# Performance work log

Measured on AMD Instinct MI355X. Metric: run time of the kernel, lower is better.

The kernel has to match this reference:

```python
import jax, jax.numpy as jnp
import numpy as np

NEG_SLOPE = 0.2


def gatv2(x, src, dst, eattr, Wl, bl, Wr, br, We, att, bias, concat):
    # GATv2Conv (PyG semantics): message j->i, softmax over incoming edges of target i.
    n = x.shape[0]
    H, C = att.shape
    xl = (x @ Wl + bl).reshape(n, H, C)   # source transform lin_l
    xr = (x @ Wr + br).reshape(n, H, C)   # target transform lin_r
    xe = (eattr @ We).reshape(-1, H, C)   # edge transform lin_edge (no bias)
    g = jax.nn.leaky_relu(xl[src] + xr[dst] + xe, NEG_SLOPE)  # [E,H,C]
    e = jnp.einsum('ehc,hc->eh', g, att)                      # [E,H]
    m = jax.ops.segment_max(e, dst, num_segments=n)
    a = jnp.exp(e - m[dst])
    s = jax.ops.segment_sum(a, dst, num_segments=n)
    alpha = a / (s[dst] + 1e-16)                              # [E,H]
    out = jax.ops.segment_sum(alpha[:, :, None] * xl[src], dst, num_segments=n)
    out = out.reshape(n, H * C) if concat else out.mean(axis=1)
    return out + bias, alpha


def add_self_loops(src, dst, eattr, n):
    # PyG default: add_self_loops=True, fill_value='mean' for edge_attr
    loop = jnp.arange(n, dtype=src.dtype)
    fill = jnp.broadcast_to(eattr.mean(axis=0, keepdims=True), (n, eattr.shape[1]))
    return (jnp.concatenate([src, loop]), jnp.concatenate([dst, loop]),
            jnp.concatenate([eattr, fill], axis=0))


def setup_inputs() -> dict:
    key = jax.random.key(0)
    ks = iter(jax.random.split(key, 64))
    B, N, D = 4, 2048, 256
    n = B * N
    E = 131072
    H, C1 = 4, 64  # conv1: heads=4, out=hidden//heads=64 (concat -> 256)
    C2 = 256       # conv2: heads=4, out=256, concat=False (mean)
    IN1 = 770

    def rn(shape, s=0.05):
        return jax.random.normal(next(ks), shape, dtype=jnp.float32) * s

    inp = {
        'h': rn((B, N, D), 1.0), 'c_temp': rn((B, N, D), 1.0),
        'c_stereo': rn((B, N, D), 1.0), 'e_proj': rn((B, N, 2), 1.0),
        'f_Lt': rn((B, N, D), 1.0),
        'edges': jax.random.randint(next(ks), (2, E), 0, n, dtype=jnp.int64),
        'edge_attr': rn((E, 1), 1.0),
        # conv1
        'Wl1': rn((IN1, H * C1)), 'bl1': jnp.zeros((H * C1,), jnp.float32),
        'Wr1': rn((IN1, H * C1)), 'br1': jnp.zeros((H * C1,), jnp.float32),
        'We1': rn((1, H * C1)), 'att1': rn((H, C1)),
        'bias1': jnp.zeros((H * C1,), jnp.float32),
        # conv2
        'Wl2': rn((D, H * C2)), 'bl2': jnp.zeros((H * C2,), jnp.float32),
        'Wr2': rn((D, H * C2)), 'br2': jnp.zeros((H * C2,), jnp.float32),
        'We2': rn((1, H * C2)), 'att2': rn((H, C2)),
        'bias2': jnp.zeros((C2,), jnp.float32),
        # GRUCell ([in, 3H] layout; gate order r,z,n as in torch)
        'Wih': rn((D, 3 * D)), 'bih': jnp.zeros((3 * D,), jnp.float32),
        'Whh': rn((D, 3 * D)), 'bhh': jnp.zeros((3 * D,), jnp.float32),
        # heads
        'rW1': rn((D, 256)), 'rb1': jnp.zeros((256,), jnp.float32),
        'rW2': rn((256, 2)), 'rb2': jnp.zeros((2,), jnp.float32),
        'wW1': rn((D, 256)), 'wb1': jnp.zeros((256,), jnp.float32),
        'wW2': rn((256, 2)), 'wb2': jnp.zeros((2,), jnp.float32),
        'pW1': rn((D, 128)), 'pb1': jnp.zeros((128,), jnp.float32),
        'pW2': rn((128, 1)), 'pb2': jnp.zeros((1,), jnp.float32),
        'dW1': rn((D, 128)), 'db1': jnp.zeros((128,), jnp.float32),
        'dW2': rn((128, 1)), 'db2': jnp.zeros((1,), jnp.float32),
    }
    return inp


def reference(h, c_temp, c_stereo, e_proj, f_Lt, edges, edge_attr,
              Wl1, bl1, Wr1, br1, We1, att1, bias1,
              Wl2, bl2, Wr2, br2, We2, att2, bias2,
              Wih, bih, Whh, bhh,
              rW1, rb1, rW2, rb2, wW1, wb1, wW2, wb2,
              pW1, pb1, pW2, pb2, dW1, db1, dW2, db2):
    B, N, D = f_Lt.shape
    n = B * N
    x = jnp.concatenate([c_temp, c_stereo, e_proj, f_Lt], axis=-1).reshape(n, -1)

    src, dst, ea = add_self_loops(edges[0], edges[1], edge_attr, n)
    x1, _ = gatv2(x, src, dst, ea, Wl1, bl1, Wr1, br1, We1, att1, bias1, concat=True)
    x1 = jax.nn.relu(x1)
    x2, alpha = gatv2(x1, src, dst, ea, Wl2, bl2, Wr2, br2, We2, att2, bias2, concat=False)

    # GRUCell
    hf = h.reshape(n, -1)
    gi = x2 @ Wih + bih
    gh = hf @ Whh + bhh
    ir, iz, inew = jnp.split(gi, 3, axis=-1)
    hr, hz, hnew = jnp.split(gh, 3, axis=-1)
    r_g = jax.nn.sigmoid(ir + hr)
    z_g = jax.nn.sigmoid(iz + hz)
    n_g = jnp.tanh(inew + r_g * hnew)
    h_new = ((1.0 - z_g) * n_g + z_g * hf).reshape(B, N, D)

    res = jax.nn.relu(h_new @ rW1 + rb1) @ rW2 + rb2
    w = jax.nn.sigmoid(jax.nn.relu(h_new @ wW1 + wb1) @ wW2 + wb2)
    a_p = jax.nn.softplus(jax.nn.relu(h_new @ pW1 + pb1) @ pW2 + pb2).mean(axis=1)
    a_d = jax.nn.softplus(jax.nn.relu(h_new @ dW1 + db1) @ dW2 + db2)
    return (h_new, res, w, a_p, a_d)
```

## Files before the change

kernel.cpp:

```cpp
#include <hip/hip_runtime.h>
#include <hip/hip_bf16.h>
#include <cstdint>
#include <cstddef>

#define N_NODES 8192
#define E_RAW   131072
#define E_TOT   (E_RAW + N_NODES)
#define HEADS   4

typedef __attribute__((ext_vector_type(8))) __bf16 bf16x8;
typedef __attribute__((ext_vector_type(4))) float f32x4;
typedef __attribute__((ext_vector_type(2))) float f32x2;

__device__ __forceinline__ void gload_lds16(const void* g, void* lds) {
  __builtin_amdgcn_global_load_lds(
      (const __attribute__((address_space(1))) unsigned int*)g,
      (__attribute__((address_space(3))) unsigned int*)lds, 16, 0, 0);
}

__device__ __forceinline__ float bfbits2f(unsigned short u) {
  return __uint_as_float((unsigned)u << 16);
}
__device__ __forceinline__ unsigned short f2bfbits(float f) {
  __hip_bfloat16 b = __float2bfloat16(f);
  return *(unsigned short*)&b;
}
__device__ __forceinline__ f32x2 unpk2(unsigned u) {
  return (f32x2){__uint_as_float(u << 16), __uint_as_float(u & 0xffff0000u)};
}
__device__ __forceinline__ unsigned char f32_to_fp8(float v) {
  int r = __builtin_amdgcn_cvt_pk_fp8_f32(v, v, 0, false);
  return (unsigned char)(r & 0xff);
}

__device__ __forceinline__ int eSrc(const int* __restrict__ src, int e) {
  return (e < E_RAW) ? src[e] : (e - E_RAW);
}
__device__ __forceinline__ int eDst(const int* __restrict__ dst, int e) {
  return (e < E_RAW) ? dst[e] : (e - E_RAW);
}


__global__ __launch_bounds__(256) void prep_kernel(
    const float* __restrict__ ct, const float* __restrict__ cs,
    const float* __restrict__ ep, const float* __restrict__ fl,
    const float* __restrict__ h, const float* __restrict__ ea,
    const float* bl1, const float* br1, const float* bl2, const float* br2,
    const float* rb1, const float* wb1, const float* pb1, const float* db1,
    __hip_bfloat16* __restrict__ x, __hip_bfloat16* __restrict__ Hb,
    float* __restrict__ MP, int* __restrict__ icnt_ipos,
    float* B1, float* B2, float* BH) {
  int blk = blockIdx.x;
  int tid = threadIdx.x;
  if (blk < 8192) {
    int i = blk;
    for (int j = tid; j < 832; j += 256) {
      float v;
      if (j < 256)      v = ct[(size_t)i * 256 + j];
      else if (j < 512) v = cs[(size_t)i * 256 + (j - 256)];
      else if (j < 514) v = ep[(size_t)i * 2 + (j - 512)];
      else if (j < 770) v = fl[(size_t)i * 256 + (j - 514)];
      else              v = 0.f;
      x[(size_t)i * 832 + j] = __float2bfloat16(v);
    }
  } else if (blk < 9216) {
    size_t base = ((size_t)(blk - 8192) * 256 + tid) * 8;
    float4 a = *(const float4*)(h + base);
    float4 b = *(const float4*)(h + base + 4);
    unsigned short o[8];
    o[0]=f2bfbits(a.x); o[1]=f2bfbits(a.y); o[2]=f2bfbits(a.z); o[3]=f2bfbits(a.w);
    o[4]=f2bfbits(b.x); o[5]=f2bfbits(b.y); o[6]=f2bfbits(b.z); o[7]=f2bfbits(b.w);
    *(uint4*)((unsigned short*)Hb + base) = *(uint4*)o;
  } else if (blk < 9472) {
    __shared__ float sm[256];
    int bb = blk - 9216;
    float acc = 0.f;
    for (int i = bb * 256 + tid; i < E_RAW; i += 256 * 256) acc += ea[i];
    sm[tid] = acc; __syncthreads();
    for (int s = 128; s; s >>= 1) { if (tid < s) sm[tid] += sm[tid + s]; __syncthreads(); }
    if (tid == 0) MP[bb] = sm[0];
  } else if (blk < 9536) {
    int i = (blk - 9472) * 256 + tid;
    if (i < 2 * N_NODES) icnt_ipos[i] = 0;
  } else {
    int i = (blk - 9536) * 256 + tid;
    if (i < 512) B1[i] = (i < 256) ? bl1[i] : br1[i - 256];
    else if (i < 2560) { int k = i - 512; B2[k] = (k < 1024) ? bl2[k] : br2[k - 1024]; }
    else if (i < 3328) {
      int k = i - 2560;
      BH[k] = (k < 256) ? rb1[k] : (k < 512) ? wb1[k - 256] : (k < 640) ? pb1[k - 512] : db1[k - 640];
    }
  }
}


__global__ void csr_count(const int* __restrict__ dst, int* __restrict__ cnt) {
  int e = blockIdx.x * blockDim.x + threadIdx.x;
  if (e < E_TOT) atomicAdd(&cnt[eDst(dst, e)], 1);
}

__global__ __launch_bounds__(1024) void csr_scan(const int* __restrict__ cnt,
                                                 int* __restrict__ off,
                                                 float* __restrict__ MP) {
  __shared__ int part[1024];
  __shared__ float sm[256];
  int t = threadIdx.x;
  if (t < 256) sm[t] = MP[t];
  __syncthreads();
  for (int s = 128; s; s >>= 1) { if (t < s) sm[t] += sm[t + s]; __syncthreads(); }
  if (t == 0) MP[256] = sm[0] * (1.f / (float)E_RAW);
  int base = t * 8;
  int loc[8];
  int s = 0;
#pragma unroll
  for (int i = 0; i < 8; ++i) { loc[i] = s; s += cnt[base + i]; }
  part[t] = s; __syncthreads();
  for (int d = 1; d < 1024; d <<= 1) {
    int v = (t >= d) ? part[t - d] : 0;
    __syncthreads();
    part[t] += v;
    __syncthreads();
  }
  int pre = (t == 0) ? 0 : part[t - 1];
#pragma unroll
  for (int i = 0; i < 8; ++i) off[base + i] = pre + loc[i];
  if (t == 1023) off[8192] = part[1023];
}

__global__ void csr_fill(const int* __restrict__ src, const int* __restrict__ dst,
                         const float* __restrict__ ea, const float* __restrict__ eamean,
                         const int* __restrict__ off, int* __restrict__ pos,
                         int* __restrict__ srcn, float* __restrict__ eav) {
  int e = blockIdx.x * blockDim.x + threadIdx.x;
  if (e >= E_TOT) return;
  int d = eDst(dst, e);
  int p = off[d] + atomicAdd(&pos[d], 1);
  srcn[p] = eSrc(src, e);
  eav[p] = (e < E_RAW) ? ea[e] : eamean[0];
}


__global__ __launch_bounds__(256) void wt_all(
    const float* w0, const float* w1, const float* w2, const float* w3,
    const float* w4, const float* w5, const float* w6, const float* w7,
    const float* w8, const float* w9,
    __hip_bfloat16* WT1, __hip_bfloat16* WT2, __hip_bfloat16* WTih,
    __hip_bfloat16* WThh, __hip_bfloat16* WTh) {
  const int cum[10] = {208, 416, 672, 928, 1120, 1312, 1376, 1440, 1472, 1504};
  const int Kt[10]  = {770, 770, 256, 256, 256, 256, 256, 256, 256, 256};
  const int Nt[10]  = {256, 256, 1024, 1024, 768, 768, 256, 256, 128, 128};
  const int KPt[10] = {832, 832, 256, 256, 256, 256, 256, 256, 256, 256};
  const int n0t[10] = {0, 256, 0, 1024, 0, 0, 0, 256, 512, 640};
  int job = 0;
  while (blockIdx.x >= (unsigned)cum[job]) ++job;
  int lb = blockIdx.x - (job ? cum[job - 1] : 0);
  int K = Kt[job], N = Nt[job], KP = KPt[job], n0 = n0t[job];
  int tilesX = KP >> 5;
  int k0 = (lb % tilesX) * 32, nb = (lb / tilesX) * 32;
  const float* W;
  switch (job) {
    case 0: W = w0; break; case 1: W = w1; break; case 2: W = w2; break;
    case 3: W = w3; break; case 4: W = w4; break; case 5: W = w5; break;
    case 6: W = w6; break; case 7: W = w7; break; case 8: W = w8; break;
    default: W = w9; break;
  }
  __hip_bfloat16* WT = (job < 2) ? WT1 : (job < 4) ? WT2 : (job == 4) ? WTih
                       : (job == 5) ? WThh : WTh;
  __shared__ float sm[32][33];
  int tx = threadIdx.x & 31, ty = threadIdx.x >> 5;
  for (int yy = ty; yy < 32; yy += 8) {
    int k = k0 + yy, n = nb + tx;
    sm[yy][tx] = (k < K && n < N) ? W[(size_t)k * N + n] : 0.f;
  }
  __syncthreads();
  for (int yy = ty; yy < 32; yy += 8) {
    int n = nb + yy, k = k0 + tx;
    if (n < N) WT[(size_t)(n0 + n) * KP + k] = __float2bfloat16(sm[tx][yy]);
  }
}


template <int OUT>
__global__ __launch_bounds__(512) void mfma_gemm(
    const __hip_bfloat16* __restrict__ A, const __hip_bfloat16* __restrict__ BT,
    const float* __restrict__ bias, void* __restrict__ Cout, int KP, int N,
    unsigned char* __restrict__ Cfp8) {
  __shared__ uint4 AsBuf[1024];
  __shared__ uint4 BsBuf[1024];
  char* Asc = (char*)AsBuf;
  char* Bsc = (char*)BsBuf;
  int tid = threadIdx.x;
  int lane = tid & 63;
  int wid = tid >> 6;
  int wr = wid >> 1;
  int wc = wid & 1;
  int bm = blockIdx.y * 128;
  int bn = blockIdx.x * 128;
  f32x4 acc[2][4];
#pragma unroll
  for (int i = 0; i < 2; ++i)
#pragma unroll
    for (int j = 0; j < 4; ++j) acc[i][j] = (f32x4){0.f, 0.f, 0.f, 0.f};

  int nK = KP >> 6;
  for (int kt = 0; kt < nK; ++kt) {
    int k0 = kt * 64;
#pragma unroll
    for (int i = 0; i < 2; ++i) {
      int p = i * 512 + tid;
      int row = p >> 3, cc = p & 7;
      int sc = cc ^ (row & 7);
      gload_lds16(A + (size_t)(bm + row) * KP + k0 + sc * 8, Asc + p * 16);
      gload_lds16(BT + (size_t)(bn + row) * KP + k0 + sc * 8, Bsc + p * 16);
    }
    __syncthreads();
#pragma unroll
    for (int s = 0; s < 2; ++s) {
      bf16x8 af[2], bfr[4];
#pragma unroll
      for (int f = 0; f < 2; ++f) {
        int r = wr * 32 + f * 16 + (lane & 15);
        int ch = (s * 4 + (lane >> 4)) ^ (r & 7);
        af[f] = *(const bf16x8*)(Asc + r * 128 + ch * 16);
      }
#pragma unroll
      for (int f = 0; f < 4; ++f) {
        int n = wc * 64 + f * 16 + (lane & 15);
        int cb = (s * 4 + (lane >> 4)) ^ (n & 7);
        bfr[f] = *(const bf16x8*)(Bsc + n * 128 + cb * 16);
      }
#pragma unroll
      for (int fm = 0; fm < 2; ++fm)
#pragma unroll
        for (int fn = 0; fn < 4; ++fn)
          acc[fm][fn] = __builtin_amdgcn_mfma_f32_16x16x32_bf16(af[fm], bfr[fn], acc[fm][fn], 0, 0, 0);
    }
    __syncthreads();
  }
  int rbase = bm + wr * 32 + (lane >> 4) * 4;
  int cbase = bn + wc * 64 + (lane & 15);
#pragma unroll
  for (int fm = 0; fm < 2; ++fm)
#pragma unroll
    for (int fn = 0; fn < 4; ++fn) {
      int col = cbase + fn * 16;
      float bv = bias[col];
#pragma unroll
      for (int j = 0; j < 4; ++j) {
        int row = rbase + fm * 16 + j;
        float v = acc[fm][fn][j] + bv;
        if (OUT == 3) v = fmaxf(v, 0.f);
        if (OUT == 0 || OUT == 3)
          ((__hip_bfloat16*)Cout)[(size_t)row * N + col] = __float2bfloat16(v);
        if (OUT == 6) {
          if (col < 256) Cfp8[(size_t)row * 256 + col] = f32_to_fp8(v);
          else ((__hip_bfloat16*)Cout)[(size_t)row * N + col] = __float2bfloat16(v);
        }
        if (OUT == 7) {
          if (col < 1024) Cfp8[(size_t)row * 1024 + col] = f32_to_fp8(v);
          else ((__hip_bfloat16*)Cout)[(size_t)row * N + col] = __float2bfloat16(v);
        }
      }
    }
}


__global__ __launch_bounds__(256) void gat_fused1(
    const unsigned char* __restrict__ XL8,
    const __hip_bfloat16* __restrict__ XLR,
    const int* __restrict__ off, const int* __restrict__ srcn,
    const float* __restrict__ eav, const float* __restrict__ We,
    const float* __restrict__ att, const float* __restrict__ bias,
    __hip_bfloat16* __restrict__ X1) {
  int d = (blockIdx.x * 256 + threadIdx.x) >> 6;
  int lane = threadIdx.x & 63;
  int q = lane & 15;
  int j0 = (lane >> 4) * 64 + q * 4;
  const unsigned short* X = (const unsigned short*)XLR;
  uint2 xv = *(const uint2*)(X + (size_t)d * 512 + 256 + j0);
  f32x2 xr[2] = {unpk2(xv.x), unpk2(xv.y)};
  f32x2 we[2] = {*(const f32x2*)(We + j0), *(const f32x2*)(We + j0 + 2)};
  f32x2 at[2] = {*(const f32x2*)(att + j0), *(const f32x2*)(att + j0 + 2)};
  int b = off[d], e1 = off[d + 1], pe = e1 - 1;
  int sB = srcn[b]; float eaA = eav[b];
  unsigned rA = *(const unsigned*)(XL8 + (size_t)sB * 256 + j0);
  int p1 = min(b + 1, pe); sB = srcn[p1]; float eaB = eav[p1];
  float m = -INFINITY, ss = 0.f;
  f32x2 a[2] = {(f32x2){0.f, 0.f}, (f32x2){0.f, 0.f}};
  for (int p = b; p < e1; ++p) {
    unsigned cc = rA; float ea = eaA; eaA = eaB;
    rA = *(const unsigned*)(XL8 + (size_t)sB * 256 + j0);
    int p2 = min(p + 2, pe); sB = srcn[p2]; eaB = eav[p2];
    f32x2 v[2];
    v[0] = (f32x2){__builtin_amdgcn_cvt_f32_fp8(cc, 0), __builtin_amdgcn_cvt_f32_fp8(cc, 1)};
    v[1] = (f32x2){__builtin_amdgcn_cvt_f32_fp8(cc, 2), __builtin_amdgcn_cvt_f32_fp8(cc, 3)};
    f32x2 ea2 = (f32x2){ea, ea};
    f32x2 t2 = (f32x2){0.f, 0.f};
#pragma unroll
    for (int i = 0; i < 2; ++i) {
      f32x2 gg = (v[i] + xr[i]) + ea2 * we[i];
      f32x2 lr = __builtin_elementwise_max(gg, 0.2f * gg);
      t2 = t2 + lr * at[i];
    }
    float t = t2.x + t2.y;
    t += __shfl_xor(t, 8, 64); t += __shfl_xor(t, 4, 64);
    t += __shfl_xor(t, 2, 64); t += __shfl_xor(t, 1, 64);
    if (__all(t <= m)) {
      float wp = __expf(t - m);
      ss += wp;
      f32x2 wp2 = (f32x2){wp, wp};
#pragma unroll
      for (int i = 0; i < 2; ++i) a[i] = a[i] + wp2 * v[i];
    } else {
      float mn = fmaxf(m, t);
      float scl = __expf(m - mn);
      float wp = __expf(t - mn);
      ss = fmaf(ss, scl, wp);
      f32x2 wp2 = (f32x2){wp, wp}, s2 = (f32x2){scl, scl};
#pragma unroll
      for (int i = 0; i < 2; ++i) a[i] = a[i] * s2 + wp2 * v[i];
      m = mn;
    }
  }
  float inv = 1.f / (ss + 1e-16f);
  unsigned short o[4];
  o[0] = f2bfbits(fmaxf(fmaf(a[0].x, inv, bias[j0]), 0.f));
  o[1] = f2bfbits(fmaxf(fmaf(a[0].y, inv, bias[j0 + 1]), 0.f));
  o[2] = f2bfbits(fmaxf(fmaf(a[1].x, inv, bias[j0 + 2]), 0.f));
  o[3] = f2bfbits(fmaxf(fmaf(a[1].y, inv, bias[j0 + 3]), 0.f));
  *(uint2*)((unsigned short*)X1 + (size_t)d * 256 + j0) = *(uint2*)o;
}


__global__ __launch_bounds__(256) void gat_fused2(
    const unsigned char* __restrict__ XL8,
    const __hip_bfloat16* __restrict__ XLR,
    const int* __restrict__ off, const int* __restrict__ srcn,
    const float* __restrict__ eav, const float* __restrict__ We,
    const float* __restrict__ att, const float* __restrict__ bias,
    __hip_bfloat16* __restrict__ X2) {
  int d = (blockIdx.x * 256 + threadIdx.x) >> 6;
  int lane = threadIdx.x & 63;
  int g = lane >> 4, q = lane & 15;
  int j0 = g * 256 + q * 16;
  const unsigned short* X = (const unsigned short*)XLR;
  f32x2 xr[8], we[8], at[8], a[8];
  {
    const uint4* xp = (const uint4*)(X + (size_t)d * 2048 + 1024 + j0);
    uint4 r0 = xp[0], r1 = xp[1];
    xr[0] = unpk2(r0.x); xr[1] = unpk2(r0.y); xr[2] = unpk2(r0.z); xr[3] = unpk2(r0.w);
    xr[4] = unpk2(r1.x); xr[5] = unpk2(r1.y); xr[6] = unpk2(r1.z); xr[7] = unpk2(r1.w);
#pragma unroll
    for (int i = 0; i < 8; ++i) {
      we[i] = *(const f32x2*)(We + j0 + 2 * i);
      at[i] = *(const f32x2*)(att + j0 + 2 * i);
      a[i] = (f32x2){0.f, 0.f};
    }
  }
  int b = off[d], e1 = off[d + 1], pe = e1 - 1;
  int sB = srcn[b]; float eaA = eav[b];
  uint4 rA = *(const uint4*)(XL8 + (size_t)sB * 1024 + j0);
  int p1 = min(b + 1, pe); sB = srcn[p1]; float eaB = eav[p1];
  float m = -INFINITY, ss = 0.f;
  for (int p = b; p < e1; ++p) {
    uint4 cc = rA; float ea = eaA; eaA = eaB;
    rA = *(const uint4*)(XL8 + (size_t)sB * 1024 + j0);
    int p2 = min(p + 2, pe); sB = srcn[p2]; eaB = eav[p2];
    f32x2 v[8];
    v[0] = (f32x2){__builtin_amdgcn_cvt_f32_fp8(cc.x, 0), __builtin_amdgcn_cvt_f32_fp8(cc.x, 1)};
    v[1] = (f32x2){__builtin_amdgcn_cvt_f32_fp8(cc.x, 2), __builtin_amdgcn_cvt_f32_fp8(cc.x, 3)};
    v[2] = (f32x2){__builtin_amdgcn_cvt_f32_fp8(cc.y, 0), __builtin_amdgcn_cvt_f32_fp8(cc.y, 1)};
    v[3] = (f32x2){__builtin_amdgcn_cvt_f32_fp8(cc.y, 2), __builtin_amdgcn_cvt_f32_fp8(cc.y, 3)};
    v[4] = (f32x2){__builtin_amdgcn_cvt_f32_fp8(cc.z, 0), __builtin_amdgcn_cvt_f32_fp8(cc.z, 1)};
    v[5] = (f32x2){__builtin_amdgcn_cvt_f32_fp8(cc.z, 2), __builtin_amdgcn_cvt_f32_fp8(cc.z, 3)};
    v[6] = (f32x2){__builtin_amdgcn_cvt_f32_fp8(cc.w, 0), __builtin_amdgcn_cvt_f32_fp8(cc.w, 1)};
    v[7] = (f32x2){__builtin_amdgcn_cvt_f32_fp8(cc.w, 2), __builtin_amdgcn_cvt_f32_fp8(cc.w, 3)};
    f32x2 ea2 = (f32x2){ea, ea};
    f32x2 t2 = (f32x2){0.f, 0.f};
#pragma unroll
    for (int i = 0; i < 8; ++i) {
      f32x2 gg = (v[i] + xr[i]) + ea2 * we[i];
      f32x2 lr = __builtin_elementwise_max(gg, 0.2f * gg);
      t2 = t2 + lr * at[i];
    }
    float t = t2.x + t2.y;
    t += __shfl_xor(t, 8, 64); t += __shfl_xor(t, 4, 64);
    t += __shfl_xor(t, 2, 64); t += __shfl_xor(t, 1, 64);
    if (__all(t <= m)) {
      float wp = __expf(t - m);
      ss += wp;
      f32x2 wp2 = (f32x2){wp, wp};
#pragma unroll
      for (int i = 0; i < 8; ++i) a[i] = a[i] + wp2 * v[i];
    } else {
      float mn = fmaxf(m, t);
      float scl = __expf(m - mn);
      float wp = __expf(t - mn);
      ss = fmaf(ss, scl, wp);
      f32x2 wp2 = (f32x2){wp, wp}, s2 = (f32x2){scl, scl};
#pragma unroll
      for (int i = 0; i < 8; ++i) a[i] = a[i] * s2 + wp2 * v[i];
      m = mn;
    }
  }
  float inv = 1.f / (ss + 1e-16f);
  f32x2 inv2 = (f32x2){inv, inv};
#pragma unroll
  for (int i = 0; i < 8; ++i) {
    f32x2 r2 = a[i] * inv2;
    r2.x += __shfl_xor(r2.x, 16, 64);
    r2.x += __shfl_xor(r2.x, 32, 64);
    r2.y += __shfl_xor(r2.y, 16, 64);
    r2.y += __shfl_xor(r2.y, 32, 64);
    a[i] = r2;
  }
  if (g == 0) {
    unsigned short o[16];
#pragma unroll
    for (int i = 0; i < 8; ++i) {
      o[2 * i]     = f2bfbits(fmaf(0.25f, a[i].x, bias[q * 16 + 2 * i]));
      o[2 * i + 1] = f2bfbits(fmaf(0.25f, a[i].y, bias[q * 16 + 2 * i + 1]));
    }
    uint4* op = (uint4*)((unsigned short*)X2 + (size_t)d * 256 + q * 16);
    op[0] = ((uint4*)o)[0];
    op[1] = ((uint4*)o)[1];
  }
}


__global__ __launch_bounds__(512) void gru_gemm(
    const __hip_bfloat16* __restrict__ X2b,
    const __hip_bfloat16* __restrict__ Hb,
    const __hip_bfloat16* __restrict__ WTih,
    const __hip_bfloat16* __restrict__ WThh,
    const float* __restrict__ bih, const float* __restrict__ bhh,
    const float* __restrict__ hf,
    float* __restrict__ hn, __hip_bfloat16* __restrict__ hnb) {
  __shared__ uint4 AxB[512];
  __shared__ uint4 AhB[512];
  __shared__ uint4 BiB[1024];
  __shared__ uint4 BhB[1024];
  char* Ax = (char*)AxB;
  char* Ah = (char*)AhB;
  char* Bi = (char*)BiB;
  char* Bh = (char*)BhB;
  int tid = threadIdx.x;
  int lane = tid & 63, wid = tid >> 6;
  int wr = wid >> 1, wc = wid & 1;
  int bm = blockIdx.y * 64;
  int c0 = blockIdx.x * 128;
  float rv[16], zv[16];
  float outv[16];
  for (int gate = 0; gate < 3; ++gate) {
    f32x4 ai[4], ah[4];
#pragma unroll
    for (int j = 0; j < 4; ++j) { ai[j] = (f32x4){0.f,0.f,0.f,0.f}; ah[j] = (f32x4){0.f,0.f,0.f,0.f}; }
    for (int kt = 0; kt < 4; ++kt) {
      int k0 = kt * 64;
      {
        int p = tid;
        int row = p >> 3, cc = p & 7;
        int sc = cc ^ (row & 7);
        gload_lds16(X2b + (size_t)(bm + row) * 256 + k0 + sc * 8, Ax + p * 16);
        gload_lds16(Hb + (size_t)(bm + row) * 256 + k0 + sc * 8, Ah + p * 16);
      }
#pragma unroll
      for (int i = 0; i < 2; ++i) {
        int p = i * 512 + tid;
        int row = p >> 3, cc = p & 7;
        int sc = cc ^ (row & 7);
        int n = gate * 256 + c0 + row;
        gload_lds16(WTih + (size_t)n * 256 + k0 + sc * 8, Bi + p * 16);
        gload_lds16(WThh + (size_t)n * 256 + k0 + sc * 8, Bh + p * 16);
      }
      __syncthreads();
#pragma unroll
      for (int s = 0; s < 2; ++s) {
        int rl = wr * 16 + (lane & 15);
        int ch = (s * 4 + (lane >> 4)) ^ (rl & 7);
        bf16x8 axf = *(const bf16x8*)(Ax + rl * 128 + ch * 16);
        bf16x8 ahf = *(const bf16x8*)(Ah + rl * 128 + ch * 16);
        bf16x8 bif[4], bhf[4];
#pragma unroll
        for (int f = 0; f < 4; ++f) {
          int nl = wc * 64 + f * 16 + (lane & 15);
          int cb = (s * 4 + (lane >> 4)) ^ (nl & 7);
          bif[f] = *(const bf16x8*)(Bi + nl * 128 + cb * 16);
          bhf[f] = *(const bf16x8*)(Bh + nl * 128 + cb * 16);
        }
#pragma unroll
        for (int fn = 0; fn < 4; ++fn) {
          ai[fn] = __builtin_amdgcn_mfma_f32_16x16x32_bf16(axf, bif[fn], ai[fn], 0, 0, 0);
          ah[fn] = __builtin_amdgcn_mfma_f32_16x16x32_bf16(ahf, bhf[fn], ah[fn], 0, 0, 0);
        }
      }
      __syncthreads();
    }
#pragma unroll
    for (int fn = 0; fn < 4; ++fn) {
      int colL = wc * 64 + fn * 16 + (lane & 15);
      int ng = gate * 256 + c0 + colL;
      float bi_v = bih[ng], bh_v = bhh[ng];
#pragma unroll
      for (int j = 0; j < 4; ++j) {
        int k = fn * 4 + j;
        float vi = ai[fn][j] + bi_v;
        float vh = ah[fn][j] + bh_v;
        if (gate == 0) rv[k] = 1.f / (1.f + __expf(-(vi + vh)));
        else if (gate == 1) zv[k] = 1.f / (1.f + __expf(-(vi + vh)));
        else outv[k] = tanhf(vi + rv[k] * vh);
      }
    }
  }
#pragma unroll
  for (int fn = 0; fn < 4; ++fn) {
    int colL = wc * 64 + fn * 16 + (lane & 15);
    int chn = c0 + colL;
#pragma unroll
    for (int j = 0; j < 4; ++j) {
      int k = fn * 4 + j;
      int row = bm + wr * 16 + (lane >> 4) * 4 + j;
      float h0 = hf[(size_t)row * 256 + chn];
      float v = (1.f - zv[k]) * outv[k] + zv[k] * h0;
      hn[(size_t)row * 256 + chn] = v;
      hnb[(size_t)row * 256 + chn] = __float2bfloat16(v);
    }
  }
}


__global__ __launch_bounds__(256) void heads_final(
    const __hip_bfloat16* __restrict__ Tb,
    const float* __restrict__ rW2, const float* __restrict__ rb2,
    const float* __restrict__ wW2, const float* __restrict__ wb2,
    const float* __restrict__ pW2, const float* __restrict__ pb2,
    const float* __restrict__ dW2, const float* __restrict__ db2,
    float* __restrict__ o_res, float* __restrict__ o_w,
    float* __restrict__ AP, float* __restrict__ o_ad) {
  int node = (blockIdx.x * 256 + threadIdx.x) >> 6;
  int lane = threadIdx.x & 63;
  const unsigned short* t = (const unsigned short*)Tb + (size_t)node * 768;
  ushort4 tr = *(const ushort4*)(t + lane * 4);
  ushort4 tw = *(const ushort4*)(t + 256 + lane * 4);
  float trf[4] = {bfbits2f(tr.x), bfbits2f(tr.y), bfbits2f(tr.z), bfbits2f(tr.w)};
  float twf[4] = {bfbits2f(tw.x), bfbits2f(tw.y), bfbits2f(tw.z), bfbits2f(tw.w)};
  float tpf[4] = {0.f, 0.f, 0.f, 0.f}, tdf[4] = {0.f, 0.f, 0.f, 0.f};
  if (lane < 32) {
    ushort4 tp = *(const ushort4*)(t + 512 + lane * 4);
    ushort4 td = *(const ushort4*)(t + 640 + lane * 4);
    tpf[0] = bfbits2f(tp.x); tpf[1] = bfbits2f(tp.y); tpf[2] = bfbits2f(tp.z); tpf[3] = bfbits2f(tp.w);
    tdf[0] = bfbits2f(td.x); tdf[1] = bfbits2f(td.y); tdf[2] = bfbits2f(td.z); tdf[3] = bfbits2f(td.w);
  }
  float r0 = 0.f, r1 = 0.f, w0 = 0.f, w1 = 0.f, pp = 0.f, dd = 0.f;
#pragma unroll
  for (int i = 0; i < 4; ++i) {
    int k = lane * 4 + i;
    r0 = fmaf(trf[i], rW2[k * 2], r0);
    r1 = fmaf(trf[i], rW2[k * 2 + 1], r1);
    w0 = fmaf(twf[i], wW2[k * 2], w0);
    w1 = fmaf(twf[i], wW2[k * 2 + 1], w1);
  }
  if (lane < 32) {
#pragma unroll
    for (int i = 0; i < 4; ++i) {
      int k = lane * 4 + i;
      pp = fmaf(tpf[i], pW2[k], pp);
      dd = fmaf(tdf[i], dW2[k], dd);
    }
  }
#pragma unroll
  for (int o = 32; o; o >>= 1) {
    r0 += __shfl_xor(r0, o, 64); r1 += __shfl_xor(r1, o, 64);
    w0 += __shfl_xor(w0, o, 64); w1 += __shfl_xor(w1, o, 64);
    pp += __shfl_xor(pp, o, 64); dd += __shfl_xor(dd, o, 64);
  }
  if (lane == 0) {
    o_res[(size_t)node * 2]     = r0 + rb2[0];
    o_res[(size_t)node * 2 + 1] = r1 + rb2[1];
    float sw0 = w0 + wb2[0], sw1 = w1 + wb2[1];
    o_w[(size_t)node * 2]     = 1.f / (1.f + __expf(-sw0));
    o_w[(size_t)node * 2 + 1] = 1.f / (1.f + __expf(-sw1));
    float vp = pp + pb2[0];
    AP[node] = fmaxf(vp, 0.f) + log1pf(__expf(-fabsf(vp)));
    float vd = dd + db2[0];
    o_ad[node] = fmaxf(vd, 0.f) + log1pf(__expf(-fabsf(vd)));
  }
}

__global__ void ap_reduce(const float* __restrict__ ap, float* __restrict__ out) {
  __shared__ float sm[256];
  int b = blockIdx.x, tid = threadIdx.x;
  float acc = 0.f;
  for (int i = tid; i < 2048; i += 256) acc += ap[b * 2048 + i];
  sm[tid] = acc; __syncthreads();
  for (int s = 128; s; s >>= 1) { if (tid < s) sm[tid] += sm[tid + s]; __syncthreads(); }
  if (tid == 0) out[b] = sm[0] * (1.f / 2048.f);
}


extern "C" void kernel_launch(void* const* d_in, const int* in_sizes, int n_in,
                              void* d_out, int out_size, void* d_ws, size_t ws_size,
                              hipStream_t stream) {
  const float* h        = (const float*)d_in[0];
  const float* c_temp   = (const float*)d_in[1];
  const float* c_stereo = (const float*)d_in[2];
  const float* e_proj   = (const float*)d_in[3];
  const float* f_Lt     = (const float*)d_in[4];
  const int*   edges    = (const int*)d_in[5];
  const float* eattr    = (const float*)d_in[6];
  const float* Wl1 = (const float*)d_in[7];  const float* bl1 = (const float*)d_in[8];
  const float* Wr1 = (const float*)d_in[9];  const float* br1 = (const float*)d_in[10];
  const float* We1 = (const float*)d_in[11]; const float* att1 = (const float*)d_in[12];
  const float* bias1 = (const float*)d_in[13];
  const float* Wl2 = (const float*)d_in[14]; const float* bl2 = (const float*)d_in[15];
  const float* Wr2 = (const float*)d_in[16]; const float* br2 = (const float*)d_in[17];
  const float* We2 = (const float*)d_in[18]; const float* att2 = (const float*)d_in[19];
  const float* bias2 = (const float*)d_in[20];
  const float* Wih = (const float*)d_in[21]; const float* bih = (const float*)d_in[22];
  const float* Whh = (const float*)d_in[23]; const float* bhh = (const float*)d_in[24];
  const float* rW1 = (const float*)d_in[25]; const float* rb1 = (const float*)d_in[26];
  const float* rW2 = (const float*)d_in[27]; const float* rb2 = (const float*)d_in[28];
  const float* wW1 = (const float*)d_in[29]; const float* wb1 = (const float*)d_in[30];
  const float* wW2 = (const float*)d_in[31]; const float* wb2 = (const float*)d_in[32];
  const float* pW1 = (const float*)d_in[33]; const float* pb1 = (const float*)d_in[34];
  const float* pW2 = (const float*)d_in[35]; const float* pb2 = (const float*)d_in[36];
  const float* dW1 = (const float*)d_in[37]; const float* db1 = (const float*)d_in[38];
  const float* dW2 = (const float*)d_in[39]; const float* db2 = (const float*)d_in[40];

  const int* src = edges;
  const int* dst = edges + E_RAW;

  float* base = (float*)d_ws;
  size_t cur = 0;
  auto alloc = [&](size_t n) { float* p = base + cur; cur += (n + 63) & ~(size_t)63; return p; };

  float* BIG0 = alloc(8388608);
  float* BIG1 = alloc(6291456);
  float* XLR1f = alloc(2097152);
  float* XL8f = alloc(2097152);
  float* XL81f = alloc(524288);
  float* X1f  = alloc(1048576);
  float* X2f  = alloc(1048576);
  float* Hbf  = alloc(1048576);
  float* HNbf = alloc(1048576);
  float* WT1f = alloc(212992);
  float* WT2f = alloc(262144);
  float* WTihf = alloc(98304);
  float* WThhf = alloc(98304);
  float* WThf  = alloc(98304);
  float* B1 = alloc(512);
  float* B2 = alloc(2048);
  float* BH = alloc(768);
  float* EAV = alloc(E_TOT);
  float* AP  = alloc(N_NODES);
  float* MP  = alloc(320);
  int* ICNT = (int*)alloc(2 * N_NODES);
  int* IOFF = (int*)alloc(N_NODES + 64);
  int* ISRC = (int*)alloc(E_TOT);
  if (ws_size < cur * 4) return;
  int* IPOS = ICNT + N_NODES;

  __hip_bfloat16* x_bf = (__hip_bfloat16*)BIG1;
  __hip_bfloat16* XLR1 = (__hip_bfloat16*)XLR1f;
  __hip_bfloat16* XLR2 = (__hip_bfloat16*)BIG0;
  unsigned char* XL8 = (unsigned char*)XL8f;
  unsigned char* XL81 = (unsigned char*)XL81f;
  __hip_bfloat16* X1b = (__hip_bfloat16*)X1f;
  __hip_bfloat16* X2b = (__hip_bfloat16*)X2f;
  __hip_bfloat16* Hb  = (__hip_bfloat16*)Hbf;
  __hip_bfloat16* HNb = (__hip_bfloat16*)HNbf;
  __hip_bfloat16* WT1 = (__hip_bfloat16*)WT1f;
  __hip_bfloat16* WT2 = (__hip_bfloat16*)WT2f;
  __hip_bfloat16* WTih = (__hip_bfloat16*)WTihf;
  __hip_bfloat16* WThh = (__hip_bfloat16*)WThhf;
  __hip_bfloat16* WTh  = (__hip_bfloat16*)WThf;
  __hip_bfloat16* Tb = (__hip_bfloat16*)BIG0;

  float* o_hnew = (float*)d_out;
  float* o_res  = o_hnew + (size_t)N_NODES * 256;
  float* o_w    = o_res + (size_t)N_NODES * 2;
  float* o_ap   = o_w + (size_t)N_NODES * 2;
  float* o_ad   = o_ap + 4;

  prep_kernel<<<9549, 256, 0, stream>>>(c_temp, c_stereo, e_proj, f_Lt, h, eattr,
                                        bl1, br1, bl2, br2, rb1, wb1, pb1, db1,
                                        x_bf, Hb, MP, ICNT, B1, B2, BH);
  csr_count<<<(E_TOT + 255) / 256, 256, 0, stream>>>(dst, ICNT);
  csr_scan<<<1, 1024, 0, stream>>>(ICNT, IOFF, MP);
  csr_fill<<<(E_TOT + 255) / 256, 256, 0, stream>>>(src, dst, eattr, MP + 256,
                                                    IOFF, IPOS, ISRC, EAV);
  wt_all<<<1504, 256, 0, stream>>>(Wl1, Wr1, Wl2, Wr2, Wih, Whh, rW1, wW1, pW1, dW1,
                                   WT1, WT2, WTih, WThh, WTh);

  mfma_gemm<6><<<dim3(4, 64), 512, 0, stream>>>(x_bf, WT1, B1, XLR1, 832, 512, XL81);
  gat_fused1<<<N_NODES / 4, 256, 0, stream>>>(XL81, XLR1, IOFF, ISRC, EAV, We1, att1, bias1, X1b);

  mfma_gemm<7><<<dim3(16, 64), 512, 0, stream>>>(X1b, WT2, B2, XLR2, 256, 2048, XL8);
  gat_fused2<<<N_NODES / 4, 256, 0, stream>>>(XL8, XLR2, IOFF, ISRC, EAV, We2, att2, bias2, X2b);

  gru_gemm<<<dim3(2, 128), 512, 0, stream>>>(X2b, Hb, WTih, WThh, bih, bhh, h, o_hnew, HNb);

  mfma_gemm<3><<<dim3(6, 64), 512, 0, stream>>>(HNb, WTh, BH, Tb, 256, 768, nullptr);
  heads_final<<<N_NODES / 4, 256, 0, stream>>>(Tb, rW2, rb2, wW2, wb2, pW2, pb2, dW2, db2,
                                               o_res, o_w, AP, o_ad);
  ap_reduce<<<4, 256, 0, stream>>>(AP, o_ap);
}
```

Before: 201.7 us.

## Sort GAT destination nodes by in-degree and fold weight transpose into prep kernel

Builds an in-degree histogram in csr_scan and a degree-sorted node permutation in csr_fill, descending by degree. Both GAT aggregation kernels then process destinations in that order, so the warps inside a block see similar edge counts and the heaviest nodes are scheduled first. Separately, the weight-transpose kernel is merged into prep_kernel as extra blocks, which removes one launch. The cost is an extra indirection per wave, and neighbouring node outputs are no longer written together, which can hurt locality.

After: 207.6 us. +2.9%, slower.

```diff
diff --git a/kernel.cpp b/kernel.cpp
--- a/kernel.cpp
+++ b/kernel.cpp
@@ -47,9 +47,16 @@
     const float* __restrict__ h, const float* __restrict__ ea,
     const float* bl1, const float* br1, const float* bl2, const float* br2,
     const float* rb1, const float* wb1, const float* pb1, const float* db1,
+    const float* w0, const float* w1, const float* w2, const float* w3,
+    const float* w4, const float* w5, const float* w6, const float* w7,
+    const float* w8, const float* w9,
     __hip_bfloat16* __restrict__ x, __hip_bfloat16* __restrict__ Hb,
-    float* __restrict__ MP, int* __restrict__ icnt_ipos,
-    float* B1, float* B2, float* BH) {
+    float* __restrict__ MP, int* __restrict__ zero_region,
+    float* B1, float* B2, float* BH,
+    __hip_bfloat16* WT1, __hip_bfloat16* WT2, __hip_bfloat16* WTih,
+    __hip_bfloat16* WThh, __hip_bfloat16* WTh) {
+  __shared__ float sm[256];
+  __shared__ float smw[32][33];
   int blk = blockIdx.x;
   int tid = threadIdx.x;
   if (blk < 8192) {
@@ -72,24 +79,55 @@
     o[4]=f2bfbits(b.x); o[5]=f2bfbits(b.y); o[6]=f2bfbits(b.z); o[7]=f2bfbits(b.w);
     *(uint4*)((unsigned short*)Hb + base) = *(uint4*)o;
   } else if (blk < 9472) {
-    __shared__ float sm[256];
     int bb = blk - 9216;
     float acc = 0.f;
     for (int i = bb * 256 + tid; i < E_RAW; i += 256 * 256) acc += ea[i];
     sm[tid] = acc; __syncthreads();
     for (int s = 128; s; s >>= 1) { if (tid < s) sm[tid] += sm[tid + s]; __syncthreads(); }
     if (tid == 0) MP[bb] = sm[0];
-  } else if (blk < 9536) {
+  } else if (blk < 9537) {
     int i = (blk - 9472) * 256 + tid;
-    if (i < 2 * N_NODES) icnt_ipos[i] = 0;
-  } else {
-    int i = (blk - 9536) * 256 + tid;
+    if (i < 2 * N_NODES + 64) zero_region[i] = 0;
+  } else if (blk < 9550) {
+    int i = (blk - 9537) * 256 + tid;
     if (i < 512) B1[i] = (i < 256) ? bl1[i] : br1[i - 256];
     else if (i < 2560) { int k = i - 512; B2[k] = (k < 1024) ? bl2[k] : br2[k - 1024]; }
     else if (i < 3328) {
       int k = i - 2560;
       BH[k] = (k < 256) ? rb1[k] : (k < 512) ? wb1[k - 256] : (k < 640) ? pb1[k - 512] : db1[k - 640];
     }
+  } else {
+    int lb_blk = blk - 9550;
+    const int cum[10] = {208, 416, 672, 928, 1120, 1312, 1376, 1440, 1472, 1504};
+    const int Kt[10]  = {770, 770, 256, 256, 256, 256, 256, 256, 256, 256};
+    const int Nt[10]  = {256, 256, 1024, 1024, 768, 768, 256, 256, 128, 128};
+    const int KPt[10] = {832, 832, 256, 256, 256, 256, 256, 256, 256, 256};
+    const int n0t[10] = {0, 256, 0, 1024, 0, 0, 0, 256, 512, 640};
+    int job = 0;
+    while (lb_blk >= cum[job]) ++job;
+    int lb = lb_blk - (job ? cum[job - 1] : 0);
+    int K = Kt[job], N = Nt[job], KP = KPt[job], n0 = n0t[job];
+    int tilesX = KP >> 5;
+    int k0 = (lb % tilesX) * 32, nb = (lb / tilesX) * 32;
+    const float* W;
+    switch (job) {
+      case 0: W = w0; break; case 1: W = w1; break; case 2: W = w2; break;
+      case 3: W = w3; break; case 4: W = w4; break; case 5: W = w5; break;
+      case 6: W = w6; break; case 7: W = w7; break; case 8: W = w8; break;
+      default: W = w9; break;
+    }
+    __hip_bfloat16* WT = (job < 2) ? WT1 : (job < 4) ? WT2 : (job == 4) ? WTih
+                         : (job == 5) ? WThh : WTh;
+    int tx = tid & 31, ty = tid >> 5;
+    for (int yy = ty; yy < 32; yy += 8) {
+      int k = k0 + yy, n = nb + tx;
+      smw[yy][tx] = (k < K && n < N) ? W[(size_t)k * N + n] : 0.f;
+    }
+    __syncthreads();
+    for (int yy = ty; yy < 32; yy += 8) {
+      int n = nb + yy, k = k0 + tx;
+      if (n < N) WT[(size_t)(n0 + n) * KP + k] = __float2bfloat16(smw[tx][yy]);
+    }
   }
 }
 
@@ -101,20 +139,27 @@
 
 __global__ __launch_bounds__(1024) void csr_scan(const int* __restrict__ cnt,
                                                  int* __restrict__ off,
-                                                 float* __restrict__ MP) {
+                                                 float* __restrict__ MP,
+                                                 int* __restrict__ doff) {
   __shared__ int part[1024];
   __shared__ float sm[256];
+  __shared__ int hist[64];
   int t = threadIdx.x;
   if (t < 256) sm[t] = MP[t];
+  if (t < 64) hist[t] = 0;
   __syncthreads();
   for (int s = 128; s; s >>= 1) { if (t < s) sm[t] += sm[t + s]; __syncthreads(); }
   if (t == 0) MP[256] = sm[0] * (1.f / (float)E_RAW);
   int base = t * 8;
   int loc[8];
-  int s = 0;
-#pragma unroll
-  for (int i = 0; i < 8; ++i) { loc[i] = s; s += cnt[base + i]; }
-  part[t] = s; __syncthreads();
+  int acc8 = 0;
+#pragma unroll
+  for (int i = 0; i < 8; ++i) {
+    int c = cnt[base + i];
+    loc[i] = acc8; acc8 += c;
+    atomicAdd(&hist[min(c, 63)], 1);
+  }
+  part[t] = acc8; __syncthreads();
   for (int d = 1; d < 1024; d <<= 1) {
     int v = (t >= d) ? part[t - d] : 0;
     __syncthreads();
@@ -125,57 +170,33 @@
 #pragma unroll
   for (int i = 0; i < 8; ++i) off[base + i] = pre + loc[i];
   if (t == 1023) off[8192] = part[1023];
+  __syncthreads();
+  if (t == 0) {
+    int acc = 0;
+    for (int bb = 63; bb >= 0; --bb) { doff[bb] = acc; acc += hist[bb]; }
+  }
 }
 
 __global__ void csr_fill(const int* __restrict__ src, const int* __restrict__ dst,
                          const float* __restrict__ ea, const float* __restrict__ eamean,
                          const int* __restrict__ off, int* __restrict__ pos,
-                         int* __restrict__ srcn, float* __restrict__ eav) {
-  int e = blockIdx.x * blockDim.x + threadIdx.x;
-  if (e >= E_TOT) return;
-  int d = eDst(dst, e);
-  int p = off[d] + atomicAdd(&pos[d], 1);
-  srcn[p] = eSrc(src, e);
-  eav[p] = (e < E_RAW) ? ea[e] : eamean[0];
-}
-
-
-__global__ __launch_bounds__(256) void wt_all(
-    const float* w0, const float* w1, const float* w2, const float* w3,
-    const float* w4, const float* w5, const float* w6, const float* w7,
-    const float* w8, const float* w9,
-    __hip_bfloat16* WT1, __hip_bfloat16* WT2, __hip_bfloat16* WTih,
-    __hip_bfloat16* WThh, __hip_bfloat16* WTh) {
-  const int cum[10] = {208, 416, 672, 928, 1120, 1312, 1376, 1440, 1472, 1504};
-  const int Kt[10]  = {770, 770, 256, 256, 256, 256, 256, 256, 256, 256};
-  const int Nt[10]  = {256, 256, 1024, 1024, 768, 768, 256, 256, 128, 128};
-  const int KPt[10] = {832, 832, 256, 256, 256, 256, 256, 256, 256, 256};
-  const int n0t[10] = {0, 256, 0, 1024, 0, 0, 0, 256, 512, 640};
-  int job = 0;
-  while (blockIdx.x >= (unsigned)cum[job]) ++job;
-  int lb = blockIdx.x - (job ? cum[job - 1] : 0);
-  int K = Kt[job], N = Nt[job], KP = KPt[job], n0 = n0t[job];
-  int tilesX = KP >> 5;
-  int k0 = (lb % tilesX) * 32, nb = (lb / tilesX) * 32;
-  const float* W;
-  switch (job) {
-    case 0: W = w0; break; case 1: W = w1; break; case 2: W = w2; break;
-    case 3: W = w3; break; case 4: W = w4; break; case 5: W = w5; break;
-    case 6: W = w6; break; case 7: W = w7; break; case 8: W = w8; break;
-    default: W = w9; break;
-  }
-  __hip_bfloat16* WT = (job < 2) ? WT1 : (job < 4) ? WT2 : (job == 4) ? WTih
-                       : (job == 5) ? WThh : WTh;
-  __shared__ float sm[32][33];
-  int tx = threadIdx.x & 31, ty = threadIdx.x >> 5;
-  for (int yy = ty; yy < 32; yy += 8) {
-    int k = k0 + yy, n = nb + tx;
-    sm[yy][tx] = (k < K && n < N) ? W[(size_t)k * N + n] : 0.f;
-  }
-  __syncthreads();
-  for (int yy = ty; yy < 32; yy += 8) {
-    int n = nb + yy, k = k0 + tx;
-    if (n < N) WT[(size_t)(n0 + n) * KP + k] = __float2bfloat16(sm[tx][yy]);
+                         int* __restrict__ srcn, float* __restrict__ eav,
+                         const int* __restrict__ cnt, const int* __restrict__ doff,
+                         int* __restrict__ dpos, int* __restrict__ perm) {
+  int blk = blockIdx.x;
+  if (blk < 544) {
+    int e = blk * 256 + threadIdx.x;
+    if (e >= E_TOT) return;
+    int d = eDst(dst, e);
+    int p = off[d] + atomicAdd(&pos[d], 1);
+    srcn[p] = eSrc(src, e);
+    eav[p] = (e < E_RAW) ? ea[e] : eamean[0];
+  } else {
+    int i = (blk - 544) * 256 + threadIdx.x;
+    if (i >= N_NODES) return;
+    int bin = min(cnt[i], 63);
+    int p = doff[bin] + atomicAdd(&dpos[bin], 1);
+    perm[p] = i;
   }
 }
 
@@ -269,10 +290,10 @@
     const unsigned char* __restrict__ XL8,
     const __hip_bfloat16* __restrict__ XLR,
     const int* __restrict__ off, const int* __restrict__ srcn,
-    const float* __restrict__ eav, const float* __restrict__ We,
-    const float* __restrict__ att, const float* __restrict__ bias,
-    __hip_bfloat16* __restrict__ X1) {
-  int d = (blockIdx.x * 256 + threadIdx.x) >> 6;
+    const float* __restrict__ eav, const int* __restrict__ perm,
+    const float* __restrict__ We, const float* __restrict__ att,
+    const float* __restrict__ bias, __hip_bfloat16* __restrict__ X1) {
+  int d = perm[(blockIdx.x * 256 + threadIdx.x) >> 6];
   int lane = threadIdx.x & 63;
   int q = lane & 15;
   int j0 = (lane >> 4) * 64 + q * 4;
@@ -336,10 +357,10 @@
     const unsigned char* __restrict__ XL8,
     const __hip_bfloat16* __restrict__ XLR,
     const int* __restrict__ off, const int* __restrict__ srcn,
-    const float* __restrict__ eav, const float* __restrict__ We,
-    const float* __restrict__ att, const float* __restrict__ bias,
-    __hip_bfloat16* __restrict__ X2) {
-  int d = (blockIdx.x * 256 + threadIdx.x) >> 6;
+    const float* __restrict__ eav, const int* __restrict__ perm,
+    const float* __restrict__ We, const float* __restrict__ att,
+    const float* __restrict__ bias, __hip_bfloat16* __restrict__ X2) {
+  int d = perm[(blockIdx.x * 256 + threadIdx.x) >> 6];
   int lane = threadIdx.x & 63;
   int g = lane >> 4, q = lane & 15;
   int j0 = g * 256 + q * 16;
@@ -654,11 +675,14 @@
   float* EAV = alloc(E_TOT);
   float* AP  = alloc(N_NODES);
   float* MP  = alloc(320);
-  int* ICNT = (int*)alloc(2 * N_NODES);
+  int* ICNT = (int*)alloc(2 * N_NODES + 64);
   int* IOFF = (int*)alloc(N_NODES + 64);
   int* ISRC = (int*)alloc(E_TOT);
+  int* DOFF = (int*)alloc(64);
+  int* PERM = (int*)alloc(N_NODES);
   if (ws_size < cur * 4) return;
   int* IPOS = ICNT + N_NODES;
+  int* DPOS = IPOS + N_NODES;
 
   __hip_bfloat16* x_bf = (__hip_bfloat16*)BIG1;
   __hip_bfloat16* XLR1 = (__hip_bfloat16*)XLR1f;
@@ -682,21 +706,23 @@
   float* o_ap   = o_w + (size_t)N_NODES * 2;
   float* o_ad   = o_ap + 4;
 
-  prep_kernel<<<9549, 256, 0, stream>>>(c_temp, c_stereo, e_proj, f_Lt, h, eattr,
-                                        bl1, br1, bl2, br2, rb1, wb1, pb1, db1,
-                                        x_bf, Hb, MP, ICNT, B1, B2, BH);
+  prep_kernel<<<11054, 256, 0, stream>>>(c_temp, c_stereo, e_proj, f_Lt, h, eattr,
+                                         bl1, br1, bl2, br2, rb1, wb1, pb1, db1,
+                                         Wl1, Wr1, Wl2, Wr2, Wih, Whh, rW1, wW1, pW1, dW1,
+                                         x_bf, Hb, MP, ICNT, B1, B2, BH,
+                                         WT1, WT2, WTih, WThh, WTh);
   csr_count<<<(E_TOT + 255) / 256, 256, 0, stream>>>(dst, ICNT);
-  csr_scan<<<1, 1024, 0, stream>>>(ICNT, IOFF, MP);
-  csr_fill<<<(E_TOT + 255) / 256, 256, 0, stream>>>(src, dst, eattr, MP + 256,
-                                                    IOFF, IPOS, ISRC, EAV);
-  wt_all<<<1504, 256, 0, stream>>>(Wl1, Wr1, Wl2, Wr2, Wih, Whh, rW1, wW1, pW1, dW1,
-                                   WT1, WT2, WTih, WThh, WTh);
+  csr_scan<<<1, 1024, 0, stream>>>(ICNT, IOFF, MP, DOFF);
+  csr_fill<<<576, 256, 0, stream>>>(src, dst, eattr, MP + 256, IOFF, IPOS, ISRC, EAV,
+                                    ICNT, DOFF, DPOS, PERM);
 
   mfma_gemm<6><<<dim3(4, 64), 512, 0, stream>>>(x_bf, WT1, B1, XLR1, 832, 512, XL81);
-  gat_fused1<<<N_NODES / 4, 256, 0, stream>>>(XL81, XLR1, IOFF, ISRC, EAV, We1, att1, bias1, X1b);
+  gat_fused1<<<N_NODES / 4, 256, 0, stream>>>(XL81, XLR1, IOFF, ISRC, EAV, PERM,
+                                              We1, att1, bias1, X1b);
 
   mfma_gemm<7><<<dim3(16, 64), 512, 0, stream>>>(X1b, WT2, B2, XLR2, 256, 2048, XL8);
-  gat_fused2<<<N_NODES / 4, 256, 0, stream>>>(XL8, XLR2, IOFF, ISRC, EAV, We2, att2, bias2, X2b);
+  gat_fused2<<<N_NODES / 4, 256, 0, stream>>>(XL8, XLR2, IOFF, ISRC, EAV, PERM,
+                                              We2, att2, bias2, X2b);
 
   gru_gemm<<<dim3(2, 128), 512, 0, stream>>>(X2b, Hb, WTih, WThh, bih, bhh, h, o_hnew, HNb);
 
```
